# Kernel tuning notes

Measured on AMD Instinct MI355X. Metric: run time of the kernel, lower is better.

Reference implementation:

```python
import jax, jax.numpy as jnp
import numpy as np

B, NQ, NP_, D = 4, 2048, 8192, 256
T, H = 10, 4  # num_tables, num_hash_functions -> hash code length T*H = 40


def setup_inputs() -> dict:
    key = jax.random.key(0)
    k1, k2, k3 = jax.random.split(key, 3)
    return {
        "query_points": jax.random.normal(k1, (B, NQ, D), dtype=jnp.float32),
        "points": jax.random.normal(k2, (B, NP_, D), dtype=jnp.float32),
        "proj": jax.random.normal(k3, (T * H, D), dtype=jnp.float32),  # projection_matrices
        "k": 16,
    }


def _hash(x, proj):
    # x: [B, N, D], proj: [T*H, D] -> binary hash [B, N, T*H]
    return (jnp.einsum('bnd,fd->bnf', x, proj) > 0).astype(jnp.float32)


def reference(query_points, points, proj, k):
    qh = _hash(query_points, proj)   # [B, Nq, F]
    ph = _hash(points, proj)         # [B, Np, F]
    # L1 cdist on {0,1}-valued vectors == Hamming: |a-b| = a + b - 2ab (exact in fp32).
    sq = qh.sum(-1)                  # [B, Nq]
    sp = ph.sum(-1)                  # [B, Np]
    dist = sq[:, :, None] + sp[:, None, :] - 2.0 * jnp.einsum('bqf,bpf->bqp', qh, ph)
    kk = min(int(k), points.shape[1])
    neg_vals, indices = jax.lax.top_k(-dist, kk)  # smallest-k distances
    return indices, -neg_vals
```

## Files before the change

### kernel.cpp

```cpp
#include <hip/hip_runtime.h>
#include <stdint.h>

#define B_  4
#define NQ_ 2048
#define NP_ 8192
#define D_  256
#define F_  40
#define K_  16

__global__ __launch_bounds__(256) void hash_kernel(
    const float* __restrict__ qp, const float* __restrict__ pp,
    const float* __restrict__ proj, uint64_t* __restrict__ qcodes,
    uint64_t* __restrict__ pcodes) {
  __shared__ float tile[64 * 257];
  int t = threadIdx.x;
  int v0 = blockIdx.x * 64;
  bool isQ = v0 < B_ * NQ_;
  const float* src =
      isQ ? (qp + (size_t)v0 * D_) : (pp + (size_t)(v0 - B_ * NQ_) * D_);

#pragma unroll 8
  for (int i = 0; i < 64; ++i) tile[i * 257 + t] = src[i * 256 + t];
  __syncthreads();

  int lane = t & 63, w = t >> 6;
  int fbase = __builtin_amdgcn_readfirstlane(w * 10);
  const float* pj = proj + (size_t)fbase * 256;

  float acc[10];
#pragma unroll
  for (int f = 0; f < 10; ++f) acc[f] = 0.0f;
#pragma unroll 4
  for (int d = 0; d < 256; ++d) {
    float x = tile[lane * 257 + d];
#pragma unroll
    for (int f = 0; f < 10; ++f) acc[f] = fmaf(x, pj[f * 256 + d], acc[f]);
  }
  unsigned bits = 0;
#pragma unroll
  for (int f = 0; f < 10; ++f)
    if (acc[f] > 0.0f) bits |= 1u << f;

  __syncthreads();
  unsigned short* cb = (unsigned short*)tile;
  cb[lane * 4 + w] = (unsigned short)bits;
  __syncthreads();
  if (w == 0) {
    uint64_t code = (uint64_t)cb[lane * 4 + 0] |
                    ((uint64_t)cb[lane * 4 + 1] << 10) |
                    ((uint64_t)cb[lane * 4 + 2] << 20) |
                    ((uint64_t)cb[lane * 4 + 3] << 30);
    int gv = v0 + lane;
    if (isQ) qcodes[gv] = code;
    else pcodes[gv - B_ * NQ_] = code;
  }
}

__global__ __launch_bounds__(1024) void select_kernel(
    const uint64_t* __restrict__ qcodes, const uint64_t* __restrict__ pcodes,
    float* __restrict__ outIdx, float* __restrict__ outDist) {
  __shared__ ulonglong2 ldsP2[NP_ / 2];
  __shared__ unsigned keybuf[16][K_];
  uint64_t* ldsP = (uint64_t*)ldsP2;

  int tid = threadIdx.x;
  int bb = blockIdx.x >> 7;
  const ulonglong2* pb2 = (const ulonglong2*)(pcodes + (size_t)bb * NP_);
  for (int i = tid; i < NP_ / 2; i += 1024) ldsP2[i] = pb2[i];
  __syncthreads();

  int w = tid >> 6, lane = tid & 63;
  int qg = blockIdx.x * 16 + w;
  uint64_t qc = qcodes[qg];
  const uint64_t M = 0x00FF00FF00FF00FFull;

  unsigned pack[16];
#pragma unroll
  for (int i = 0; i < 16; ++i) pack[i] = 0;
  uint64_t cf = 0;
#pragma unroll
  for (int j2 = 0; j2 < 64; ++j2) {
    ulonglong2 pc = ldsP2[j2 * 64 + lane];
    unsigned d0 = (unsigned)__popcll(qc ^ pc.x);
    unsigned d1 = (unsigned)__popcll(qc ^ pc.y);
    unsigned c0 = d0 < 15u ? d0 : 15u;
    unsigned c1 = d1 < 15u ? d1 : 15u;
    pack[j2 >> 2] |= (c0 << (((2 * j2) & 7) * 4)) | (c1 << (((2 * j2 + 1) & 7) * 4));
    int r0 = (int)d0 - 8; r0 = r0 < 0 ? 0 : (r0 > 7 ? 7 : r0);
    int r1 = (int)d1 - 8; r1 = r1 < 0 ? 0 : (r1 > 7 ? 7 : r1);
    cf += (1ull << (r0 << 3)) + (1ull << (r1 << 3));
    if ((j2 & 7) == 7) __builtin_amdgcn_sched_barrier(0);
  }
  uint64_t e = cf & M, o = (cf >> 8) & M;
#pragma unroll
  for (int s = 1; s < 64; s <<= 1) {
    e += __shfl_xor(e, s);
    o += __shfl_xor(o, s);
  }

  int t = 0;
  unsigned n_lt = 0;
  int rfound = -1;
  {
    unsigned cum = 0;
#pragma unroll
    for (int r = 0; r < 8; ++r) {
      unsigned c = (unsigned)(((r & 1) ? o : e) >> ((r >> 1) * 16)) & 0xFFFFu;
      if (rfound < 0 && cum + c >= K_) { rfound = r; t = 8 + r; n_lt = cum; }
      cum += c;
    }
  }
  uint64_t lmask = (1ull << lane) - 1;

  if (rfound >= 1 && rfound <= 6) {
    unsigned r_need = K_ - n_lt;
    unsigned cl = 0, ce = 0;
    unsigned ut = (unsigned)t;
#pragma unroll
    for (int j2 = 0; j2 < 64; ++j2) {
      unsigned pw = pack[j2 >> 2];
      unsigned d0 = (pw >> (((2 * j2) & 7) * 4)) & 0xFu;
      unsigned d1 = (pw >> (((2 * j2 + 1) & 7) * 4)) & 0xFu;
      int p0 = j2 * 128 + 2 * lane;
      uint64_t m0 = __ballot(d0 < ut);
      uint64_t m1 = __ballot(d1 < ut);
      if (m0 | m1) {
        unsigned base =
            cl + (unsigned)__popcll(m0 & lmask) + (unsigned)__popcll(m1 & lmask);
        if (d0 < ut) keybuf[w][base] = (d0 << 13) | (unsigned)p0;
        if (d1 < ut)
          keybuf[w][base + (unsigned)((m0 >> lane) & 1)] =
              (d1 << 13) | (unsigned)(p0 + 1);
        cl += (unsigned)__popcll(m0) + (unsigned)__popcll(m1);
      }
      if (ce < r_need) {
        uint64_t q0 = __ballot(d0 == ut);
        uint64_t q1 = __ballot(d1 == ut);
        if (q0 | q1) {
          unsigned b2 =
              ce + (unsigned)__popcll(q0 & lmask) + (unsigned)__popcll(q1 & lmask);
          unsigned pos1 = b2 + (unsigned)((q0 >> lane) & 1);
          if (d0 == ut && b2 < r_need)
            keybuf[w][n_lt + b2] = (ut << 13) | (unsigned)p0;
          if (d1 == ut && pos1 < r_need)
            keybuf[w][n_lt + pos1] = (ut << 13) | (unsigned)(p0 + 1);
          ce += (unsigned)__popcll(q0) + (unsigned)__popcll(q1);
        }
      }
    }
  } else {
    uint64_t c8 = 0;
#pragma unroll 4
    for (int j = 0; j < 64; ++j) {
      ulonglong2 pc = ldsP2[j * 64 + lane];
      int d0 = __popcll(qc ^ pc.x);
      int d1 = __popcll(qc ^ pc.y);
      c8 += (1ull << (d0 & 56)) + (1ull << (d1 & 56));
    }
    uint64_t e2 = c8 & M, o2 = (c8 >> 8) & M;
#pragma unroll
    for (int s = 1; s < 64; s <<= 1) {
      e2 += __shfl_xor(e2, s);
      o2 += __shfl_xor(o2, s);
    }
    int Bb = 0;
    unsigned nbefore = 0, cum = 0;
    bool found = false;
#pragma unroll
    for (int k2 = 0; k2 < 6; ++k2) {
      unsigned c = (unsigned)(((k2 & 1) ? o2 : e2) >> ((k2 >> 1) * 16)) & 0xFFFFu;
      if (!found && cum + c >= K_) { Bb = k2; nbefore = cum; found = true; }
      cum += c;
    }
    int base = Bb * 8;
    uint64_t cff = 0;
#pragma unroll 4
    for (int j = 0; j < 64; ++j) {
      ulonglong2 pc = ldsP2[j * 64 + lane];
      unsigned r0 = (unsigned)(__popcll(qc ^ pc.x) - base);
      unsigned r1 = (unsigned)(__popcll(qc ^ pc.y) - base);
      if (r0 < 8u) cff += 1ull << (r0 << 3);
      if (r1 < 8u) cff += 1ull << (r1 << 3);
    }
    uint64_t ef = cff & M, of = (cff >> 8) & M;
#pragma unroll
    for (int s = 1; s < 64; s <<= 1) {
      ef += __shfl_xor(ef, s);
      of += __shfl_xor(of, s);
    }
    unsigned cum2 = nbefore;
    bool f2 = false;
#pragma unroll
    for (int r = 0; r < 8; ++r) {
      unsigned c = (unsigned)(((r & 1) ? of : ef) >> ((r >> 1) * 16)) & 0xFFFFu;
      if (!f2 && cum2 + c >= K_) { t = base + r; n_lt = cum2; f2 = true; }
      cum2 += c;
    }
    unsigned r_need = K_ - n_lt;
    unsigned cl = 0, ce = 0;
    for (int j = 0; j < 128; ++j) {
      int p = j * 64 + lane;
      int d = __popcll(qc ^ ldsP[p]);
      if (__any(d <= t)) {
        bool blt = (d < t), beq = (d == t);
        uint64_t mlt = __ballot(blt), meq = __ballot(beq);
        if (blt)
          keybuf[w][cl + (unsigned)__popcll(mlt & lmask)] =
              ((unsigned)d << 13) | (unsigned)p;
        if (beq) {
          unsigned pos = ce + (unsigned)__popcll(meq & lmask);
          if (pos < r_need)
            keybuf[w][n_lt + pos] = ((unsigned)d << 13) | (unsigned)p;
        }
        cl += (unsigned)__popcll(mlt);
        ce += (unsigned)__popcll(meq);
      }
    }
  }
  __syncthreads();

  if (lane < K_) {
    unsigned my = keybuf[w][lane];
    int rank = 0;
#pragma unroll
    for (int jj = 0; jj < K_; ++jj) rank += (keybuf[w][jj] < my) ? 1 : 0;
    int off = qg * K_ + rank;
    outIdx[off]  = (float)(my & 8191u);
    outDist[off] = (float)(my >> 13);
  }
}

extern "C" void kernel_launch(void* const* d_in, const int* in_sizes, int n_in,
                              void* d_out, int out_size, void* d_ws, size_t ws_size,
                              hipStream_t stream) {
  const float* qp   = (const float*)d_in[0];
  const float* pp   = (const float*)d_in[1];
  const float* proj = (const float*)d_in[2];

  uint64_t* pcodes = (uint64_t*)d_ws;
  uint64_t* qcodes = pcodes + (size_t)B_ * NP_;

  float* outIdx  = (float*)d_out;
  float* outDist = outIdx + (size_t)B_ * NQ_ * K_;

  int total_vecs = B_ * (NQ_ + NP_);
  hash_kernel<<<total_vecs / 64, 256, 0, stream>>>(qp, pp, proj, qcodes, pcodes);
  select_kernel<<<B_ * NQ_ / 16, 1024, 0, stream>>>(qcodes, pcodes, outIdx, outDist);
}
```

Measured before the change: 163.0 us.

## Stream point codes from global and spill packed distances to per-wave LDS

Drops the block-wide LDS staging of the 64KB point-code array. Each wave now reads the codes directly from global memory, relying on L1/L2 caching, and stores its packed 4-bit clamped distances in a per-wave LDS region instead of 16 registers. Blocks shrink to 512 threads (8 queries) with a launch bound of 8 waves per EU, and the trailing __syncthreads is removed since keybuf is now per-wave. The aim is to cut register pressure and LDS footprint and remove the staging barrier so occupancy rises, at the cost of repeated global/L2 reads of the point codes.

```diff
diff --git a/kernel.cpp b/kernel.cpp
--- a/kernel.cpp
+++ b/kernel.cpp
@@ -56,40 +56,38 @@
   }
 }
 
-__global__ __launch_bounds__(1024) void select_kernel(
+__global__ __launch_bounds__(512, 8) void select_kernel(
     const uint64_t* __restrict__ qcodes, const uint64_t* __restrict__ pcodes,
     float* __restrict__ outIdx, float* __restrict__ outDist) {
-  __shared__ ulonglong2 ldsP2[NP_ / 2];
-  __shared__ unsigned keybuf[16][K_];
-  uint64_t* ldsP = (uint64_t*)ldsP2;
+  __shared__ unsigned nib[8 * 1024];
+  __shared__ unsigned keybuf[8][K_];
 
   int tid = threadIdx.x;
-  int bb = blockIdx.x >> 7;
+  int w = tid >> 6, lane = tid & 63;
+  int qg = blockIdx.x * 8 + w;
+  int bb = blockIdx.x >> 8;
   const ulonglong2* pb2 = (const ulonglong2*)(pcodes + (size_t)bb * NP_);
-  for (int i = tid; i < NP_ / 2; i += 1024) ldsP2[i] = pb2[i];
-  __syncthreads();
-
-  int w = tid >> 6, lane = tid & 63;
-  int qg = blockIdx.x * 16 + w;
   uint64_t qc = qcodes[qg];
+  unsigned* nibw = nib + w * 1024;
   const uint64_t M = 0x00FF00FF00FF00FFull;
 
-  unsigned pack[16];
-#pragma unroll
-  for (int i = 0; i < 16; ++i) pack[i] = 0;
   uint64_t cf = 0;
-#pragma unroll
+  unsigned accum = 0;
+#pragma unroll 4
   for (int j2 = 0; j2 < 64; ++j2) {
-    ulonglong2 pc = ldsP2[j2 * 64 + lane];
+    ulonglong2 pc = pb2[j2 * 64 + lane];
     unsigned d0 = (unsigned)__popcll(qc ^ pc.x);
     unsigned d1 = (unsigned)__popcll(qc ^ pc.y);
     unsigned c0 = d0 < 15u ? d0 : 15u;
     unsigned c1 = d1 < 15u ? d1 : 15u;
-    pack[j2 >> 2] |= (c0 << (((2 * j2) & 7) * 4)) | (c1 << (((2 * j2 + 1) & 7) * 4));
+    accum |= (c0 | (c1 << 4)) << (8 * (j2 & 3));
     int r0 = (int)d0 - 8; r0 = r0 < 0 ? 0 : (r0 > 7 ? 7 : r0);
     int r1 = (int)d1 - 8; r1 = r1 < 0 ? 0 : (r1 > 7 ? 7 : r1);
     cf += (1ull << (r0 << 3)) + (1ull << (r1 << 3));
-    if ((j2 & 7) == 7) __builtin_amdgcn_sched_barrier(0);
+    if ((j2 & 3) == 3) {
+      nibw[lane + 64 * (j2 >> 2)] = accum;
+      accum = 0;
+    }
   }
   uint64_t e = cf & M, o = (cf >> 8) & M;
 #pragma unroll
@@ -116,43 +114,47 @@
     unsigned r_need = K_ - n_lt;
     unsigned cl = 0, ce = 0;
     unsigned ut = (unsigned)t;
-#pragma unroll
-    for (int j2 = 0; j2 < 64; ++j2) {
-      unsigned pw = pack[j2 >> 2];
-      unsigned d0 = (pw >> (((2 * j2) & 7) * 4)) & 0xFu;
-      unsigned d1 = (pw >> (((2 * j2 + 1) & 7) * 4)) & 0xFu;
-      int p0 = j2 * 128 + 2 * lane;
-      uint64_t m0 = __ballot(d0 < ut);
-      uint64_t m1 = __ballot(d1 < ut);
-      if (m0 | m1) {
-        unsigned base =
-            cl + (unsigned)__popcll(m0 & lmask) + (unsigned)__popcll(m1 & lmask);
-        if (d0 < ut) keybuf[w][base] = (d0 << 13) | (unsigned)p0;
-        if (d1 < ut)
-          keybuf[w][base + (unsigned)((m0 >> lane) & 1)] =
-              (d1 << 13) | (unsigned)(p0 + 1);
-        cl += (unsigned)__popcll(m0) + (unsigned)__popcll(m1);
-      }
-      if (ce < r_need) {
-        uint64_t q0 = __ballot(d0 == ut);
-        uint64_t q1 = __ballot(d1 == ut);
-        if (q0 | q1) {
-          unsigned b2 =
-              ce + (unsigned)__popcll(q0 & lmask) + (unsigned)__popcll(q1 & lmask);
-          unsigned pos1 = b2 + (unsigned)((q0 >> lane) & 1);
-          if (d0 == ut && b2 < r_need)
-            keybuf[w][n_lt + b2] = (ut << 13) | (unsigned)p0;
-          if (d1 == ut && pos1 < r_need)
-            keybuf[w][n_lt + pos1] = (ut << 13) | (unsigned)(p0 + 1);
-          ce += (unsigned)__popcll(q0) + (unsigned)__popcll(q1);
+#pragma unroll 4
+    for (int k = 0; k < 16; ++k) {
+      unsigned dw = nibw[lane + 64 * k];
+#pragma unroll
+      for (int b = 0; b < 4; ++b) {
+        unsigned d0 = (dw >> (8 * b)) & 0xFu;
+        unsigned d1 = (dw >> (8 * b + 4)) & 0xFu;
+        int p0 = (4 * k + b) * 128 + 2 * lane;
+        uint64_t m0 = __ballot(d0 < ut);
+        uint64_t m1 = __ballot(d1 < ut);
+        if (m0 | m1) {
+          unsigned base = cl + (unsigned)__popcll(m0 & lmask) +
+                          (unsigned)__popcll(m1 & lmask);
+          if (d0 < ut) keybuf[w][base] = (d0 << 13) | (unsigned)p0;
+          if (d1 < ut)
+            keybuf[w][base + (unsigned)((m0 >> lane) & 1)] =
+                (d1 << 13) | (unsigned)(p0 + 1);
+          cl += (unsigned)__popcll(m0) + (unsigned)__popcll(m1);
+        }
+        if (ce < r_need) {
+          uint64_t q0 = __ballot(d0 == ut);
+          uint64_t q1 = __ballot(d1 == ut);
+          if (q0 | q1) {
+            unsigned b2 = ce + (unsigned)__popcll(q0 & lmask) +
+                          (unsigned)__popcll(q1 & lmask);
+            unsigned pos1 = b2 + (unsigned)((q0 >> lane) & 1);
+            if (d0 == ut && b2 < r_need)
+              keybuf[w][n_lt + b2] = (ut << 13) | (unsigned)p0;
+            if (d1 == ut && pos1 < r_need)
+              keybuf[w][n_lt + pos1] = (ut << 13) | (unsigned)(p0 + 1);
+            ce += (unsigned)__popcll(q0) + (unsigned)__popcll(q1);
+          }
         }
       }
     }
   } else {
+    const uint64_t* pbl = pcodes + (size_t)bb * NP_;
     uint64_t c8 = 0;
 #pragma unroll 4
     for (int j = 0; j < 64; ++j) {
-      ulonglong2 pc = ldsP2[j * 64 + lane];
+      ulonglong2 pc = pb2[j * 64 + lane];
       int d0 = __popcll(qc ^ pc.x);
       int d1 = __popcll(qc ^ pc.y);
       c8 += (1ull << (d0 & 56)) + (1ull << (d1 & 56));
@@ -176,7 +178,7 @@
     uint64_t cff = 0;
 #pragma unroll 4
     for (int j = 0; j < 64; ++j) {
-      ulonglong2 pc = ldsP2[j * 64 + lane];
+      ulonglong2 pc = pb2[j * 64 + lane];
       unsigned r0 = (unsigned)(__popcll(qc ^ pc.x) - base);
       unsigned r1 = (unsigned)(__popcll(qc ^ pc.y) - base);
       if (r0 < 8u) cff += 1ull << (r0 << 3);
@@ -200,7 +202,7 @@
     unsigned cl = 0, ce = 0;
     for (int j = 0; j < 128; ++j) {
       int p = j * 64 + lane;
-      int d = __popcll(qc ^ ldsP[p]);
+      int d = __popcll(qc ^ pbl[p]);
       if (__any(d <= t)) {
         bool blt = (d < t), beq = (d == t);
         uint64_t mlt = __ballot(blt), meq = __ballot(beq);
@@ -217,7 +219,6 @@
       }
     }
   }
-  __syncthreads();
 
   if (lane < K_) {
     unsigned my = keybuf[w][lane];
@@ -245,5 +246,5 @@
 
   int total_vecs = B_ * (NQ_ + NP_);
   hash_kernel<<<total_vecs / 64, 256, 0, stream>>>(qp, pp, proj, qcodes, pcodes);
-  select_kernel<<<B_ * NQ_ / 16, 1024, 0, stream>>>(qcodes, pcodes, outIdx, outDist);
+  select_kernel<<<B_ * NQ_ / 8, 512, 0, stream>>>(qcodes, pcodes, outIdx, outDist);
 }
```

Result: faster. 150.1 us (-7.9%).
